# Performance work log

Measured on AMD Instinct MI355X. Metric: run time of the kernel, lower is better.

The kernel has to match this reference:

```python
import jax, jax.numpy as jnp
import numpy as np

K = 20
HID = 64
NUM_CLASSES = 50
BIG = 1e10  # effectively-infinite distance for self-loop exclusion


def knn_idx(x, k):
    # x: [N, d] -> idx: [N, k] indices of k nearest neighbors in feature space (excluding self)
    sq = jnp.sum(x * x, axis=1)
    dist = sq[:, None] + sq[None, :] - 2.0 * (x @ x.T)  # [N, N]
    n = x.shape[0]
    dist = dist.at[jnp.arange(n), jnp.arange(n)].set(BIG)
    _, idx = jax.lax.top_k(-dist, k)
    return idx


def edge_conv(x, k, W, b):
    # DynamicEdgeConv: message = relu(Linear(cat[x_i, x_j - x_i])), aggr = max over k neighbors
    idx = knn_idx(x, k)                      # [N, k]
    xj = x[idx]                              # [N, k, d] neighbor gather
    xi = jnp.broadcast_to(x[:, None, :], xj.shape)
    feat = jnp.concatenate([xi, xj - xi], axis=-1)   # [N, k, 2d]
    h = jax.nn.relu(jnp.einsum('nkf,fo->nko', feat, W) + b)
    return jnp.max(h, axis=1)                # [N, out]


def setup_inputs() -> dict:
    key = jax.random.key(0)
    ks = jax.random.split(key, 16)
    def lin(kw, fan_in, fan_out):
        s = 1.0 / np.sqrt(fan_in)
        return jax.random.uniform(kw, (fan_in, fan_out), jnp.float32, -s, s)
    inp = {
        'x':  jax.random.normal(ks[0], (8192, 3), jnp.float32),
        'W1': lin(ks[1], 2 * 3, HID),      'b1': jnp.zeros((HID,), jnp.float32),
        'W2': lin(ks[2], 2 * HID, HID),    'b2': jnp.zeros((HID,), jnp.float32),
        'W3': lin(ks[3], 2 * HID, HID),    'b3': jnp.zeros((HID,), jnp.float32),
        'Wl': lin(ks[4], 3 * HID, 1024),   'bl': jnp.zeros((1024,), jnp.float32),
        'Wm1': lin(ks[5], 1024, 256),      'bm1': jnp.zeros((256,), jnp.float32),
        'Wm2': lin(ks[6], 256, 128),       'bm2': jnp.zeros((128,), jnp.float32),
        'Wo': lin(ks[7], 128, NUM_CLASSES),'bo': jnp.zeros((NUM_CLASSES,), jnp.float32),
    }
    return inp


def reference(x, W1, b1, W2, b2, W3, b3, Wl, bl, Wm1, bm1, Wm2, bm2, Wo, bo):
    x1 = edge_conv(x, K, W1, b1)     # [N, 64], kNN on raw 3-D points
    x2 = edge_conv(x1, K, W2, b2)    # [N, 64], kNN recomputed in feature space
    x3 = edge_conv(x2, K, W3, b3)    # [N, 64]
    h = jnp.concatenate([x1, x2, x3], axis=1)            # [N, 192]
    h = jax.nn.relu(h @ Wl + bl)                         # lin1: MLP([192, 1024])
    h = jax.nn.relu(h @ Wm1 + bm1)                       # MLP([1024, 256]) (dropout: eval mode)
    h = jax.nn.relu(h @ Wm2 + bm2)                       # MLP([256, 128])
    out = h @ Wo + bo                                    # final Linear
    return jax.nn.log_softmax(out, axis=-1)
```

## Files before the change

kernel.cpp:

```cpp
#include <hip/hip_runtime.h>
#include <math.h>

#define NPTS 8192
#define KNN 20
#define KPART 12
#define NLISTS 32

#define OFF_SQ   0
#define OFF_IDX  8192
#define OFF_A    172032
#define OFF_B    696320
#define OFF_CAT  1220608
#define OFF_H1   2793472
#define OFF_H2   11182080
#define OFF_H3   13279232
#define OFF_PART OFF_H1
#define OFF_PACK (OFF_H1 + 5242880)
#define PACK_ELEMS 262144
#define OFF_WT   OFF_A

typedef __attribute__((ext_vector_type(8))) short bf16x8;
typedef __attribute__((ext_vector_type(16))) float f32x16;

__device__ inline unsigned umed3(unsigned a, unsigned b, unsigned c) {
    unsigned d;
    asm("v_med3_u32 %0, %1, %2, %3" : "=v"(d) : "v"(a), "v"(b), "v"(c));
    return d;
}

__device__ inline unsigned short f2bf(float f) {
    unsigned u = __float_as_uint(f);
    u += 0x7FFFu + ((u >> 16) & 1u);
    return (unsigned short)(u >> 16);
}

__device__ inline void tsplit(float x, unsigned short& hi, unsigned short& lo) {
    unsigned u = __float_as_uint(x);
    hi = (unsigned short)(u >> 16);
    float d = x - __uint_as_float(u & 0xFFFF0000u);
    lo = (unsigned short)(__float_as_uint(d) >> 16);
}

__global__ __launch_bounds__(256)
void setup_kernel(const float* __restrict__ x, float* __restrict__ sq,
                  unsigned short* __restrict__ Xhi, unsigned short* __restrict__ Xlo,
                  unsigned short* __restrict__ Yhi, unsigned short* __restrict__ Ylo) {
    const int b = blockIdx.x;
    if (b < 256) {
        int t = (b * 256 + threadIdx.x) * 2;
        int n = t >> 4, k = t & 15;
        float xv[2];
        xv[0] = (k < 3) ? x[(size_t)n * 3 + k] : 0.f;
        xv[1] = (k + 1 < 3) ? x[(size_t)n * 3 + k + 1] : 0.f;
        ushort2 hx, lx, hy, ly;
        unsigned short* hxp = (unsigned short*)&hx;
        unsigned short* lxp = (unsigned short*)&lx;
        unsigned short* hyp = (unsigned short*)&hy;
        unsigned short* lyp = (unsigned short*)&ly;
        #pragma unroll
        for (int e = 0; e < 2; ++e) {
            float xx = xv[e];
            unsigned short hi = f2bf(xx);
            float hif = __uint_as_float((unsigned)hi << 16);
            unsigned short lo = f2bf(xx - hif);
            float y = -2.f * xx;
            unsigned short yhi = f2bf(y);
            float yhif = __uint_as_float((unsigned)yhi << 16);
            unsigned short ylo = f2bf(y - yhif);
            hxp[e] = hi; lxp[e] = lo; hyp[e] = yhi; lyp[e] = ylo;
        }
        *(ushort2*)&Xhi[t] = hx;
        *(ushort2*)&Xlo[t] = lx;
        *(ushort2*)&Yhi[t] = hy;
        *(ushort2*)&Ylo[t] = ly;
    } else {
        int n = (b - 256) * 256 + threadIdx.x;
        float a = x[(size_t)n * 3], bb = x[(size_t)n * 3 + 1], c = x[(size_t)n * 3 + 2];
        sq[n] = fmaf(a, a, fmaf(bb, bb, c * c));
    }
}

__global__ __launch_bounds__(256)
void wprep_kernel(const float* __restrict__ Wl, const float* __restrict__ Wm1,
                  const float* __restrict__ Wm2,
                  unsigned short* __restrict__ WlT_hi, unsigned short* __restrict__ WlT_lo,
                  unsigned short* __restrict__ Wm1T_hi, unsigned short* __restrict__ Wm1T_lo,
                  unsigned short* __restrict__ Wm2T_hi, unsigned short* __restrict__ Wm2T_lo) {
    const int b = blockIdx.x;
    const float* W; unsigned short *Thi, *Tlo; int t, K, nmask, nbits;
    if (b < 768)       { W = Wl;  Thi = WlT_hi;  Tlo = WlT_lo;  t = b * 256 + threadIdx.x;          K = 192;  nbits = 10; }
    else if (b < 1792) { W = Wm1; Thi = Wm1T_hi; Tlo = Wm1T_lo; t = (b - 768) * 256 + threadIdx.x;  K = 1024; nbits = 8; }
    else               { W = Wm2; Thi = Wm2T_hi; Tlo = Wm2T_lo; t = (b - 1792) * 256 + threadIdx.x; K = 256;  nbits = 7; }
    nmask = (1 << nbits) - 1;
    int k = t >> nbits, n = t & nmask;
    float xx = W[t];
    unsigned short hi = f2bf(xx);
    float hif = __uint_as_float((unsigned)hi << 16);
    unsigned short lo = f2bf(xx - hif);
    Thi[(size_t)n * K + k] = hi;
    Tlo[(size_t)n * K + k] = lo;
}

#define NETP(key)                                                              \
    do {                                                                       \
        _Pragma("unroll")                                                      \
        for (int p = KPART - 1; p >= 1; --p)                                   \
            top[p] = umed3(key, top[p - 1], top[p]);                           \
        top[0] = min(top[0], key);                                             \
    } while (0)

#define PROCESS(Cv, j0base)                                                    \
    do {                                                                       \
        _Pragma("unroll")                                                      \
        for (int q = 0; q < 4; ++q) {                                          \
            _Pragma("unroll")                                                  \
            for (int t = 0; t < 4; ++t) {                                      \
                const int j = (j0base) + h * 4 + q * 8 + t;                    \
                float dd = fmaxf((Cv)[q * 4 + t], 0.f);                        \
                unsigned key = (__float_as_uint(dd) & 0xFFFFE000u) | (unsigned)j; \
                if (j == bi) key = 0xFFFFFFFFu;                                \
                NETP(key);                                                     \
            }                                                                  \
        }                                                                      \
    } while (0)

template<int KP>
__global__ __launch_bounds__(256, 2)
void knnA_mfma(const unsigned short* __restrict__ Yhi, const unsigned short* __restrict__ Ylo,
               const unsigned short* __restrict__ Xhi, const unsigned short* __restrict__ Xlo,
               const float* __restrict__ sq, unsigned int* __restrict__ part) {
    constexpr int NS = KP / 16;
    constexpr int NT = 8;
    const int wave = threadIdx.x >> 6, lane = threadIdx.x & 63;
    const int col = lane & 31;
    const int h   = lane >> 5;
    const int bi  = (blockIdx.x * 4 + wave) * 32 + col;
    const int jbase = blockIdx.y * 256;

    bf16x8 bhi[NS], blo[NS];
    #pragma unroll
    for (int s = 0; s < NS; ++s) {
        bhi[s] = *(const bf16x8*)&Xhi[(size_t)bi * KP + s * 16 + h * 8];
        blo[s] = *(const bf16x8*)&Xlo[(size_t)bi * KP + s * 16 + h * 8];
    }
    const float sqi = sq[bi];

    unsigned top[KPART];
    #pragma unroll
    for (int k = 0; k < KPART; ++k) top[k] = 0xFFFFFFFFu;

    bf16x8 fA[NS], fB[NS], lo[NS];
    f32x16 CCa, CCb;

    {
        const size_t a0 = (size_t)(jbase + col) * KP + h * 8;
        #pragma unroll
        for (int s = 0; s < NS; ++s)
            fA[s] = *(const bf16x8*)&Yhi[a0 + s * 16];
    }

    #pragma unroll 1
    for (int jt2 = 0; jt2 < NT; jt2 += 2) {
        const int j0 = jbase + jt2 * 32;
        const int aj = j0 + col;

        #pragma unroll
        for (int s = 0; s < NS; ++s)
            fB[s] = *(const bf16x8*)&Yhi[(size_t)(aj + 32) * KP + s * 16 + h * 8];
        #pragma unroll
        for (int s = 0; s < NS; ++s)
            lo[s] = *(const bf16x8*)&Ylo[(size_t)aj * KP + s * 16 + h * 8];
        float4 e0 = *(const float4*)&sq[j0 + h * 4];
        float4 e1 = *(const float4*)&sq[j0 + h * 4 + 8];
        float4 e2 = *(const float4*)&sq[j0 + h * 4 + 16];
        float4 e3 = *(const float4*)&sq[j0 + h * 4 + 24];

        if (jt2 > 0) PROCESS(CCb, j0 - 32);

        CCa[0] = sqi + e0.x; CCa[1] = sqi + e0.y; CCa[2]  = sqi + e0.z; CCa[3]  = sqi + e0.w;
        CCa[4] = sqi + e1.x; CCa[5] = sqi + e1.y; CCa[6]  = sqi + e1.z; CCa[7]  = sqi + e1.w;
        CCa[8] = sqi + e2.x; CCa[9] = sqi + e2.y; CCa[10] = sqi + e2.z; CCa[11] = sqi + e2.w;
        CCa[12] = sqi + e3.x; CCa[13] = sqi + e3.y; CCa[14] = sqi + e3.z; CCa[15] = sqi + e3.w;
        #pragma unroll
        for (int s = 0; s < NS; ++s) {
            CCa = __builtin_amdgcn_mfma_f32_32x32x16_bf16(fA[s], bhi[s], CCa, 0, 0, 0);
            CCa = __builtin_amdgcn_mfma_f32_32x32x16_bf16(fA[s], blo[s], CCa, 0, 0, 0);
            CCa = __builtin_amdgcn_mfma_f32_32x32x16_bf16(lo[s], bhi[s], CCa, 0, 0, 0);
        }

        if (jt2 + 2 < NT) {
            #pragma unroll
            for (int s = 0; s < NS; ++s)
                fA[s] = *(const bf16x8*)&Yhi[(size_t)(aj + 64) * KP + s * 16 + h * 8];
        }
        #pragma unroll
        for (int s = 0; s < NS; ++s)
            lo[s] = *(const bf16x8*)&Ylo[(size_t)(aj + 32) * KP + s * 16 + h * 8];
        float4 o0 = *(const float4*)&sq[j0 + 32 + h * 4];
        float4 o1 = *(const float4*)&sq[j0 + 32 + h * 4 + 8];
        float4 o2 = *(const float4*)&sq[j0 + 32 + h * 4 + 16];
        float4 o3 = *(const float4*)&sq[j0 + 32 + h * 4 + 24];

        PROCESS(CCa, j0);

        CCb[0] = sqi + o0.x; CCb[1] = sqi + o0.y; CCb[2]  = sqi + o0.z; CCb[3]  = sqi + o0.w;
        CCb[4] = sqi + o1.x; CCb[5] = sqi + o1.y; CCb[6]  = sqi + o1.z; CCb[7]  = sqi + o1.w;
        CCb[8] = sqi + o2.x; CCb[9] = sqi + o2.y; CCb[10] = sqi + o2.z; CCb[11] = sqi + o2.w;
        CCb[12] = sqi + o3.x; CCb[13] = sqi + o3.y; CCb[14] = sqi + o3.z; CCb[15] = sqi + o3.w;
        #pragma unroll
        for (int s = 0; s < NS; ++s) {
            CCb = __builtin_amdgcn_mfma_f32_32x32x16_bf16(fB[s], bhi[s], CCb, 0, 0, 0);
            CCb = __builtin_amdgcn_mfma_f32_32x32x16_bf16(fB[s], blo[s], CCb, 0, 0, 0);
            CCb = __builtin_amdgcn_mfma_f32_32x32x16_bf16(lo[s], bhi[s], CCb, 0, 0, 0);
        }
    }
    PROCESS(CCb, jbase + (NT - 1) * 32);

    {
        bool done = false;
        #pragma unroll
        for (int k = 0; k < KPART; ++k) {
            unsigned c = __shfl_xor(top[k], 32);
            if (!done) done = __all(c >= top[KPART - 1]);
            if (!done) NETP(c);
        }
    }

    if (h == 0) {
        unsigned* o = part + ((size_t)bi * NLISTS + blockIdx.y) * KPART;
        #pragma unroll
        for (int k = 0; k < KPART; ++k) o[k] = top[k];
    }
}

template<int D>
__global__ __launch_bounds__(256)
void knnBfeat_kernel(const unsigned int* __restrict__ part, int* __restrict__ idx_out,
                     const float* __restrict__ X, int stride, const float* __restrict__ W,
                     float* __restrict__ A, float* __restrict__ B) {
    const int wave = threadIdx.x >> 6, lane = threadIdx.x & 63;
    if (blockIdx.x < 1024) {
        const int half = lane >> 5;
        const int l = lane & 31;
        const int row = (blockIdx.x * 4 + wave) * 2 + half;

        unsigned top[KNN];
        const unsigned* p = part + ((size_t)row * NLISTS + l) * KPART;
        #pragma unroll
        for (int k = 0; k < KPART; k += 4) {
            uint4 v = *(const uint4*)(p + k);
            top[k] = v.x; top[k + 1] = v.y; top[k + 2] = v.z; top[k + 3] = v.w;
        }
        #pragma unroll
        for (int k = KPART; k < KNN; ++k) top[k] = 0xFFFFFFFFu;

        #pragma unroll
        for (int mi = 0; mi < 5; ++mi) {
            const int m = 1 << mi;
            bool done = false;
            #pragma unroll
            for (int k = 0; k < KNN; ++k) {
                unsigned c = __shfl_xor(top[k], m);
                if (!done) done = __all(c >= top[KNN - 1]);
                if (!done) {
                    #pragma unroll
                    for (int q = KNN - 1; q >= 1; --q)
                        top[q] = umed3(c, top[q - 1], top[q]);
                    top[0] = min(top[0], c);
                }
            }
        }

        if (l == 0) {
            #pragma unroll
            for (int k = 0; k < KNN; ++k)
                idx_out[(size_t)row * KNN + k] = (int)(top[k] & 0x1FFFu);
        }
    } else {
        const int n = (blockIdx.x - 1024) * 4 + wave;
        float a = 0.f, b = 0.f;
        const float* xp = X + (size_t)n * stride;
        #pragma unroll
        for (int f = 0; f < D; ++f) {
            float xf = xp[f];
            a = fmaf(xf, W[(size_t)f * 64 + lane], a);
            b = fmaf(xf, W[(size_t)(D + f) * 64 + lane], b);
        }
        A[(size_t)n * 64 + lane] = a;
        B[(size_t)n * 64 + lane] = b;
    }
}

template<bool PACKS>
__global__ __launch_bounds__(256)
void edge_fuse_kernel(const float* __restrict__ A, const float* __restrict__ B,
                      const int* __restrict__ idx, const float* __restrict__ bias,
                      float* __restrict__ out, int colofs,
                      unsigned short* __restrict__ catHi, unsigned short* __restrict__ catLo,
                      float* __restrict__ sqo,
                      unsigned short* __restrict__ Xhi, unsigned short* __restrict__ Xlo,
                      unsigned short* __restrict__ Yhi, unsigned short* __restrict__ Ylo) {
    const int wave = threadIdx.x >> 6, lane = threadIdx.x & 63;
    const int n = blockIdx.x * 4 + wave;
    const float base = A[(size_t)n * 64 + lane] - B[(size_t)n * 64 + lane] + bias[lane];
    float m = -INFINITY;
    #pragma unroll 4
    for (int k = 0; k < KNN; ++k) {
        int j = idx[(size_t)n * KNN + k];
        m = fmaxf(m, base + B[(size_t)j * 64 + lane]);
    }
    m = fmaxf(m, 0.f);
    if constexpr (PACKS) out[(size_t)n * 192 + colofs + lane] = m;

    unsigned short chi, clo;
    tsplit(m, chi, clo);
    catHi[(size_t)n * 192 + colofs + lane] = chi;
    catLo[(size_t)n * 192 + colofs + lane] = clo;

    if constexpr (PACKS) {
        float s = m * m;
        #pragma unroll
        for (int off = 32; off; off >>= 1) s += __shfl_xor(s, off);
        if (lane == 0) sqo[n] = s;

        unsigned short hi = f2bf(m);
        float hif = __uint_as_float((unsigned)hi << 16);
        unsigned short lo = f2bf(m - hif);
        float y = -2.f * m;
        unsigned short yhi = f2bf(y);
        float yhif = __uint_as_float((unsigned)yhi << 16);
        unsigned short ylo = f2bf(y - yhif);
        Xhi[(size_t)n * 64 + lane] = hi;
        Xlo[(size_t)n * 64 + lane] = lo;
        Yhi[(size_t)n * 64 + lane] = yhi;
        Ylo[(size_t)n * 64 + lane] = ylo;
    }
}

template<int K, int N, int CTW, bool SPLIT_OUT>
__global__ __launch_bounds__(256, 3)
void gemm_mfma(const unsigned short* __restrict__ Ahi, const unsigned short* __restrict__ Alo,
               const unsigned short* __restrict__ Whi, const unsigned short* __restrict__ Wlo,
               const float* __restrict__ bias, float* __restrict__ C,
               unsigned short* __restrict__ Chi, unsigned short* __restrict__ Clo) {
    const int wave = threadIdx.x >> 6, lane = threadIdx.x & 63;
    const int col = lane & 31, h = lane >> 5;
    const int r0 = blockIdx.x * 32;
    const int nb = blockIdx.y * (CTW * 128) + wave * (CTW * 32);
    const size_t abase = (size_t)(r0 + col) * K + h * 8;

    f32x16 acc[CTW];
    #pragma unroll
    for (int c = 0; c < CTW; ++c)
        #pragma unroll
        for (int r = 0; r < 16; ++r) acc[c][r] = 0.f;

    #pragma unroll 4
    for (int s = 0; s < K / 16; ++s) {
        bf16x8 ahi = *(const bf16x8*)&Ahi[abase + s * 16];
        bf16x8 alo = *(const bf16x8*)&Alo[abase + s * 16];
        #pragma unroll
        for (int c = 0; c < CTW; ++c) {
            const size_t wb = (size_t)(nb + c * 32 + col) * K + s * 16 + h * 8;
            bf16x8 bhi = *(const bf16x8*)&Whi[wb];
            bf16x8 blo = *(const bf16x8*)&Wlo[wb];
            acc[c] = __builtin_amdgcn_mfma_f32_32x32x16_bf16(ahi, bhi, acc[c], 0, 0, 0);
            acc[c] = __builtin_amdgcn_mfma_f32_32x32x16_bf16(alo, bhi, acc[c], 0, 0, 0);
            acc[c] = __builtin_amdgcn_mfma_f32_32x32x16_bf16(ahi, blo, acc[c], 0, 0, 0);
        }
    }

    #pragma unroll
    for (int c = 0; c < CTW; ++c) {
        const int n = nb + c * 32 + col;
        const float b = bias[n];
        #pragma unroll
        for (int q = 0; q < 4; ++q)
            #pragma unroll
            for (int t = 0; t < 4; ++t) {
                const int rl = 4 * h + 8 * q + t;
                float v = fmaxf(acc[c][q * 4 + t] + b, 0.f);
                if constexpr (SPLIT_OUT) {
                    unsigned short vh, vl;
                    tsplit(v, vh, vl);
                    Chi[(size_t)(r0 + rl) * N + n] = vh;
                    Clo[(size_t)(r0 + rl) * N + n] = vl;
                } else {
                    C[(size_t)(r0 + rl) * N + n] = v;
                }
            }
    }
}

__global__ __launch_bounds__(256)
void final_kernel(const float* __restrict__ H, const float* __restrict__ Wo,
                  const float* __restrict__ bo, float* __restrict__ out) {
    const int wave = threadIdx.x >> 6, lane = threadIdx.x & 63;
    const int n = blockIdx.x * 4 + wave;
    float v = -INFINITY;
    if (lane < 50) {
        float a = bo[lane];
        const float* h = H + (size_t)n * 128;
        #pragma unroll 4
        for (int f = 0; f < 128; ++f) a = fmaf(h[f], Wo[f * 50 + lane], a);
        v = a;
    }
    float mx = v;
    #pragma unroll
    for (int off = 32; off; off >>= 1) mx = fmaxf(mx, __shfl_xor(mx, off));
    float e = (lane < 50) ? expf(v - mx) : 0.f;
    float s = e;
    #pragma unroll
    for (int off = 32; off; off >>= 1) s += __shfl_xor(s, off);
    if (lane < 50) out[(size_t)n * 50 + lane] = v - mx - logf(s);
}

extern "C" void kernel_launch(void* const* d_in, const int* in_sizes, int n_in,
                              void* d_out, int out_size, void* d_ws, size_t ws_size,
                              hipStream_t stream) {
    const float* x   = (const float*)d_in[0];
    const float* W1  = (const float*)d_in[1];
    const float* b1  = (const float*)d_in[2];
    const float* W2  = (const float*)d_in[3];
    const float* b2  = (const float*)d_in[4];
    const float* W3  = (const float*)d_in[5];
    const float* b3  = (const float*)d_in[6];
    const float* Wl  = (const float*)d_in[7];
    const float* bl  = (const float*)d_in[8];
    const float* Wm1 = (const float*)d_in[9];
    const float* bm1 = (const float*)d_in[10];
    const float* Wm2 = (const float*)d_in[11];
    const float* bm2 = (const float*)d_in[12];
    const float* Wo  = (const float*)d_in[13];
    const float* bo  = (const float*)d_in[14];

    float* ws   = (float*)d_ws;
    float* sq   = ws + OFF_SQ;
    int*   idx  = (int*)(ws + OFF_IDX);
    float* Abuf = ws + OFF_A;
    float* Bbuf = ws + OFF_B;
    float* cat  = ws + OFF_CAT;
    unsigned int* part = (unsigned int*)(ws + OFF_PART);
    unsigned short* Phi = (unsigned short*)(ws + OFF_PACK);
    unsigned short* Plo = (unsigned short*)(ws + OFF_PACK + PACK_ELEMS);
    unsigned short* Qhi = (unsigned short*)(ws + OFF_PACK + 2 * PACK_ELEMS);
    unsigned short* Qlo = (unsigned short*)(ws + OFF_PACK + 3 * PACK_ELEMS);
    unsigned short* h1hi = (unsigned short*)(ws + OFF_H1);
    unsigned short* h1lo = (unsigned short*)(ws + OFF_H1 + 4194304);
    unsigned short* catHi = (unsigned short*)(ws + OFF_H2);
    unsigned short* catLo = (unsigned short*)(ws + OFF_H2 + 786432);
    unsigned short* h2hi = (unsigned short*)(ws + OFF_H2);
    unsigned short* h2lo = (unsigned short*)(ws + OFF_H2 + 1048576);
    float* h3   = ws + OFF_H3;
    unsigned short* WlT_hi  = (unsigned short*)(ws + OFF_WT);
    unsigned short* WlT_lo  = (unsigned short*)(ws + OFF_WT + 98304);
    unsigned short* Wm1T_hi = (unsigned short*)(ws + OFF_WT + 196608);
    unsigned short* Wm1T_lo = (unsigned short*)(ws + OFF_WT + 327680);
    unsigned short* Wm2T_hi = (unsigned short*)(ws + OFF_WT + 458752);
    unsigned short* Wm2T_lo = (unsigned short*)(ws + OFF_WT + 475136);
    float* out  = (float*)d_out;

    dim3 b256(256);
    dim3 gknn(64, 32);

    setup_kernel<<<288, b256, 0, stream>>>(x, sq, Phi, Plo, Qhi, Qlo);
    knnA_mfma<16><<<gknn, b256, 0, stream>>>(Qhi, Qlo, Phi, Plo, sq, part);
    knnBfeat_kernel<3><<<3072, b256, 0, stream>>>(part, idx, x, 3, W1, Abuf, Bbuf);
    edge_fuse_kernel<true><<<2048, b256, 0, stream>>>(Abuf, Bbuf, idx, b1, cat, 0,
                                                      catHi, catLo, sq, Phi, Plo, Qhi, Qlo);

    knnA_mfma<64><<<gknn, b256, 0, stream>>>(Qhi, Qlo, Phi, Plo, sq, part);
    knnBfeat_kernel<64><<<3072, b256, 0, stream>>>(part, idx, cat, 192, W2, Abuf, Bbuf);
    edge_fuse_kernel<true><<<2048, b256, 0, stream>>>(Abuf, Bbuf, idx, b2, cat, 64,
                                                      catHi, catLo, sq, Phi, Plo, Qhi, Qlo);

    knnA_mfma<64><<<gknn, b256, 0, stream>>>(Qhi, Qlo, Phi, Plo, sq, part);
    knnBfeat_kernel<64><<<3072, b256, 0, stream>>>(part, idx, cat + 64, 192, W3, Abuf, Bbuf);
    edge_fuse_kernel<false><<<2048, b256, 0, stream>>>(Abuf, Bbuf, idx, b3, cat, 128,
                                                       catHi, catLo, nullptr,
                                                       nullptr, nullptr, nullptr, nullptr);

    wprep_kernel<<<1920, b256, 0, stream>>>(Wl, Wm1, Wm2, WlT_hi, WlT_lo,
                                            Wm1T_hi, Wm1T_lo, Wm2T_hi, Wm2T_lo);

    dim3 g1(256, 4);
    gemm_mfma<192, 1024, 2, true><<<g1, b256, 0, stream>>>(catHi, catLo, WlT_hi, WlT_lo,
                                                           bl, nullptr, h1hi, h1lo);
    dim3 g2(256, 2);
    gemm_mfma<1024, 256, 1, true><<<g2, b256, 0, stream>>>(h1hi, h1lo, Wm1T_hi, Wm1T_lo,
                                                           bm1, nullptr, h2hi, h2lo);
    dim3 g3(256, 1);
    gemm_mfma<256, 128, 1, false><<<g3, b256, 0, stream>>>(h2hi, h2lo, Wm2T_hi, Wm2T_lo,
                                                           bm2, h3, nullptr, nullptr);
    final_kernel<<<2048, b256, 0, stream>>>(h3, Wo, bo, out);
}
```

Baseline: 440.1 us.

## Fuse weight prep into setup, fuse last GEMM with classifier, shrink partial top-k

Weight transpose/split is folded into the setup kernel, removing a separate launch, and the workspace is remapped so the prepared weights survive the kNN stages. The final 256->128 GEMM is fused with the 128->50 linear and log-softmax through shared memory, which drops the h3 round trip and one launch. The per-list partial top-k size drops from 12 to 10, which cuts selection work but risks missing true neighbors if more than 10 of them fall into one list. The weight split also switches from round-to-nearest to truncating tsplit.

```diff
diff --git a/kernel.cpp b/kernel.cpp
--- a/kernel.cpp
+++ b/kernel.cpp
@@ -3,7 +3,7 @@
 
 #define NPTS 8192
 #define KNN 20
-#define KPART 12
+#define KPART 10
 #define NLISTS 32
 
 #define OFF_SQ   0
@@ -13,11 +13,10 @@
 #define OFF_CAT  1220608
 #define OFF_H1   2793472
 #define OFF_H2   11182080
-#define OFF_H3   13279232
 #define OFF_PART OFF_H1
 #define OFF_PACK (OFF_H1 + 5242880)
 #define PACK_ELEMS 262144
-#define OFF_WT   OFF_A
+#define OFF_WT   (OFF_H2 + 1572864)
 
 typedef __attribute__((ext_vector_type(8))) short bf16x8;
 typedef __attribute__((ext_vector_type(16))) float f32x16;
@@ -44,10 +43,27 @@
 __global__ __launch_bounds__(256)
 void setup_kernel(const float* __restrict__ x, float* __restrict__ sq,
                   unsigned short* __restrict__ Xhi, unsigned short* __restrict__ Xlo,
-                  unsigned short* __restrict__ Yhi, unsigned short* __restrict__ Ylo) {
+                  unsigned short* __restrict__ Yhi, unsigned short* __restrict__ Ylo,
+                  const float* __restrict__ Wl, const float* __restrict__ Wm1,
+                  const float* __restrict__ Wm2,
+                  unsigned short* __restrict__ WlT_hi, unsigned short* __restrict__ WlT_lo,
+                  unsigned short* __restrict__ Wm1T_hi, unsigned short* __restrict__ Wm1T_lo,
+                  unsigned short* __restrict__ Wm2T_hi, unsigned short* __restrict__ Wm2T_lo) {
     const int b = blockIdx.x;
-    if (b < 256) {
-        int t = (b * 256 + threadIdx.x) * 2;
+    if (b < 1920) {
+        const float* W; unsigned short *Thi, *Tlo; int t, K, nbits;
+        if (b < 768)       { W = Wl;  Thi = WlT_hi;  Tlo = WlT_lo;  t = b * 256 + threadIdx.x;          K = 192;  nbits = 10; }
+        else if (b < 1792) { W = Wm1; Thi = Wm1T_hi; Tlo = Wm1T_lo; t = (b - 768) * 256 + threadIdx.x;  K = 1024; nbits = 8; }
+        else               { W = Wm2; Thi = Wm2T_hi; Tlo = Wm2T_lo; t = (b - 1792) * 256 + threadIdx.x; K = 256;  nbits = 7; }
+        int nmask = (1 << nbits) - 1;
+        int k = t >> nbits, n = t & nmask;
+        float xx = W[t];
+        unsigned short hi, lo;
+        tsplit(xx, hi, lo);
+        Thi[(size_t)n * K + k] = hi;
+        Tlo[(size_t)n * K + k] = lo;
+    } else if (b < 2176) {
+        int t = ((b - 1920) * 256 + threadIdx.x) * 2;
         int n = t >> 4, k = t & 15;
         float xv[2];
         xv[0] = (k < 3) ? x[(size_t)n * 3 + k] : 0.f;
@@ -74,31 +90,10 @@
         *(ushort2*)&Yhi[t] = hy;
         *(ushort2*)&Ylo[t] = ly;
     } else {
-        int n = (b - 256) * 256 + threadIdx.x;
+        int n = (b - 2176) * 256 + threadIdx.x;
         float a = x[(size_t)n * 3], bb = x[(size_t)n * 3 + 1], c = x[(size_t)n * 3 + 2];
         sq[n] = fmaf(a, a, fmaf(bb, bb, c * c));
     }
-}
-
-__global__ __launch_bounds__(256)
-void wprep_kernel(const float* __restrict__ Wl, const float* __restrict__ Wm1,
-                  const float* __restrict__ Wm2,
-                  unsigned short* __restrict__ WlT_hi, unsigned short* __restrict__ WlT_lo,
-                  unsigned short* __restrict__ Wm1T_hi, unsigned short* __restrict__ Wm1T_lo,
-                  unsigned short* __restrict__ Wm2T_hi, unsigned short* __restrict__ Wm2T_lo) {
-    const int b = blockIdx.x;
-    const float* W; unsigned short *Thi, *Tlo; int t, K, nmask, nbits;
-    if (b < 768)       { W = Wl;  Thi = WlT_hi;  Tlo = WlT_lo;  t = b * 256 + threadIdx.x;          K = 192;  nbits = 10; }
-    else if (b < 1792) { W = Wm1; Thi = Wm1T_hi; Tlo = Wm1T_lo; t = (b - 768) * 256 + threadIdx.x;  K = 1024; nbits = 8; }
-    else               { W = Wm2; Thi = Wm2T_hi; Tlo = Wm2T_lo; t = (b - 1792) * 256 + threadIdx.x; K = 256;  nbits = 7; }
-    nmask = (1 << nbits) - 1;
-    int k = t >> nbits, n = t & nmask;
-    float xx = W[t];
-    unsigned short hi = f2bf(xx);
-    float hif = __uint_as_float((unsigned)hi << 16);
-    unsigned short lo = f2bf(xx - hif);
-    Thi[(size_t)n * K + k] = hi;
-    Tlo[(size_t)n * K + k] = lo;
 }
 
 #define NETP(key)                                                              \
@@ -246,10 +241,13 @@
 
         unsigned top[KNN];
         const unsigned* p = part + ((size_t)row * NLISTS + l) * KPART;
-        #pragma unroll
-        for (int k = 0; k < KPART; k += 4) {
-            uint4 v = *(const uint4*)(p + k);
-            top[k] = v.x; top[k + 1] = v.y; top[k + 2] = v.z; top[k + 3] = v.w;
+        {
+            uint4 v0 = *(const uint4*)(p + 0);
+            uint4 v1 = *(const uint4*)(p + 4);
+            uint2 v2 = *(const uint2*)(p + 8);
+            top[0] = v0.x; top[1] = v0.y; top[2] = v0.z; top[3] = v0.w;
+            top[4] = v1.x; top[5] = v1.y; top[6] = v1.z; top[7] = v1.w;
+            top[8] = v2.x; top[9] = v2.y;
         }
         #pragma unroll
         for (int k = KPART; k < KNN; ++k) top[k] = 0xFFFFFFFFu;
@@ -392,27 +390,70 @@
     }
 }
 
-__global__ __launch_bounds__(256)
-void final_kernel(const float* __restrict__ H, const float* __restrict__ Wo,
-                  const float* __restrict__ bo, float* __restrict__ out) {
+__global__ __launch_bounds__(256, 2)
+void gemm3f_kernel(const unsigned short* __restrict__ Ahi, const unsigned short* __restrict__ Alo,
+                   const unsigned short* __restrict__ Whi, const unsigned short* __restrict__ Wlo,
+                   const float* __restrict__ bias,
+                   const float* __restrict__ Wo, const float* __restrict__ bo,
+                   float* __restrict__ out) {
+    constexpr int K = 256;
     const int wave = threadIdx.x >> 6, lane = threadIdx.x & 63;
-    const int n = blockIdx.x * 4 + wave;
-    float v = -INFINITY;
-    if (lane < 50) {
-        float a = bo[lane];
-        const float* h = H + (size_t)n * 128;
-        #pragma unroll 4
-        for (int f = 0; f < 128; ++f) a = fmaf(h[f], Wo[f * 50 + lane], a);
-        v = a;
-    }
-    float mx = v;
+    const int col = lane & 31, h = lane >> 5;
+    const int r0 = blockIdx.x * 32;
+    const int nb = wave * 32;
+    const size_t abase = (size_t)(r0 + col) * K + h * 8;
+
+    __shared__ float h3s[32][132];
+
+    f32x16 acc;
     #pragma unroll
-    for (int off = 32; off; off >>= 1) mx = fmaxf(mx, __shfl_xor(mx, off));
-    float e = (lane < 50) ? expf(v - mx) : 0.f;
-    float s = e;
-    #pragma unroll
-    for (int off = 32; off; off >>= 1) s += __shfl_xor(s, off);
-    if (lane < 50) out[(size_t)n * 50 + lane] = v - mx - logf(s);
+    for (int r = 0; r < 16; ++r) acc[r] = 0.f;
+
+    #pragma unroll 4
+    for (int s = 0; s < K / 16; ++s) {
+        bf16x8 ahi = *(const bf16x8*)&Ahi[abase + s * 16];
+        bf16x8 alo = *(const bf16x8*)&Alo[abase + s * 16];
+        const size_t wb = (size_t)(nb + col) * K + s * 16 + h * 8;
+        bf16x8 bhi = *(const bf16x8*)&Whi[wb];
+        bf16x8 blo = *(const bf16x8*)&Wlo[wb];
+        acc = __builtin_amdgcn_mfma_f32_32x32x16_bf16(ahi, bhi, acc, 0, 0, 0);
+        acc = __builtin_amdgcn_mfma_f32_32x32x16_bf16(alo, bhi, acc, 0, 0, 0);
+        acc = __builtin_amdgcn_mfma_f32_32x32x16_bf16(ahi, blo, acc, 0, 0, 0);
+    }
+
+    {
+        const int n = nb + col;
+        const float b = bias[n];
+        #pragma unroll
+        for (int q = 0; q < 4; ++q)
+            #pragma unroll
+            for (int t = 0; t < 4; ++t) {
+                const int rl = 4 * h + 8 * q + t;
+                h3s[rl][n] = fmaxf(acc[q * 4 + t] + b, 0.f);
+            }
+    }
+    __syncthreads();
+
+    #pragma unroll 1
+    for (int rr = 0; rr < 8; ++rr) {
+        const int row = wave * 8 + rr;
+        float v = -INFINITY;
+        if (lane < 50) {
+            float a = bo[lane];
+            #pragma unroll 4
+            for (int f = 0; f < 128; ++f)
+                a = fmaf(h3s[row][f], Wo[f * 50 + lane], a);
+            v = a;
+        }
+        float mx = v;
+        #pragma unroll
+        for (int off = 32; off; off >>= 1) mx = fmaxf(mx, __shfl_xor(mx, off));
+        float e = (lane < 50) ? expf(v - mx) : 0.f;
+        float s = e;
+        #pragma unroll
+        for (int off = 32; off; off >>= 1) s += __shfl_xor(s, off);
+        if (lane < 50) out[(size_t)(r0 + row) * 50 + lane] = v - mx - logf(s);
+    }
 }
 
 extern "C" void kernel_launch(void* const* d_in, const int* in_sizes, int n_in,
@@ -449,9 +490,8 @@
     unsigned short* h1lo = (unsigned short*)(ws + OFF_H1 + 4194304);
     unsigned short* catHi = (unsigned short*)(ws + OFF_H2);
     unsigned short* catLo = (unsigned short*)(ws + OFF_H2 + 786432);
-    unsigned short* h2hi = (unsigned short*)(ws + OFF_H2);
-    unsigned short* h2lo = (unsigned short*)(ws + OFF_H2 + 1048576);
-    float* h3   = ws + OFF_H3;
+    unsigned short* h2hi = (unsigned short*)(ws + OFF_A);
+    unsigned short* h2lo = (unsigned short*)(ws + OFF_CAT);
     unsigned short* WlT_hi  = (unsigned short*)(ws + OFF_WT);
     unsigned short* WlT_lo  = (unsigned short*)(ws + OFF_WT + 98304);
     unsigned short* Wm1T_hi = (unsigned short*)(ws + OFF_WT + 196608);
@@ -463,7 +503,10 @@
     dim3 b256(256);
     dim3 gknn(64, 32);
 
-    setup_kernel<<<288, b256, 0, stream>>>(x, sq, Phi, Plo, Qhi, Qlo);
+    setup_kernel<<<2208, b256, 0, stream>>>(x, sq, Phi, Plo, Qhi, Qlo,
+                                            Wl, Wm1, Wm2, WlT_hi, WlT_lo,
+                                            Wm1T_hi, Wm1T_lo, Wm2T_hi, Wm2T_lo);
+
     knnA_mfma<16><<<gknn, b256, 0, stream>>>(Qhi, Qlo, Phi, Plo, sq, part);
     knnBfeat_kernel<3><<<3072, b256, 0, stream>>>(part, idx, x, 3, W1, Abuf, Bbuf);
     edge_fuse_kernel<true><<<2048, b256, 0, stream>>>(Abuf, Bbuf, idx, b1, cat, 0,
@@ -479,9 +522,6 @@
     edge_fuse_kernel<false><<<2048, b256, 0, stream>>>(Abuf, Bbuf, idx, b3, cat, 128,
                                                        catHi, catLo, nullptr,
                                                        nullptr, nullptr, nullptr, nullptr);
-
-    wprep_kernel<<<1920, b256, 0, stream>>>(Wl, Wm1, Wm2, WlT_hi, WlT_lo,
-                                            Wm1T_hi, Wm1T_lo, Wm2T_hi, Wm2T_lo);
 
     dim3 g1(256, 4);
     gemm_mfma<192, 1024, 2, true><<<g1, b256, 0, stream>>>(catHi, catLo, WlT_hi, WlT_lo,
@@ -489,8 +529,6 @@
     dim3 g2(256, 2);
     gemm_mfma<1024, 256, 1, true><<<g2, b256, 0, stream>>>(h1hi, h1lo, Wm1T_hi, Wm1T_lo,
                                                            bm1, nullptr, h2hi, h2lo);
-    dim3 g3(256, 1);
-    gemm_mfma<256, 128, 1, false><<<g3, b256, 0, stream>>>(h2hi, h2lo, Wm2T_hi, Wm2T_lo,
-                                                           bm2, h3, nullptr, nullptr);
-    final_kernel<<<2048, b256, 0, stream>>>(h3, Wo, bo, out);
-}
+    gemm3f_kernel<<<256, b256, 0, stream>>>(h2hi, h2lo, Wm2T_hi, Wm2T_lo,
+                                            bm2, Wo, bo, out);
+}
```

Result: no change. 440.9 us, median of 2 (+0.2%).
